# Performance work log

Measured on AMD Instinct MI355X. Metric: run time of the kernel, lower is better.

Reference implementation:

```python
import jax, jax.numpy as jnp
import numpy as np

REG_COEF = 25.0


def setup_inputs() -> dict:
    key = jax.random.key(0)
    k1, k2, k3, k4 = jax.random.split(key, 4)
    B, C, N, RES = 32, 4, 16384, 32
    y_pred = jax.random.normal(k1, (B, C, 4), dtype=jnp.float32)
    points = jax.random.uniform(k2, (B, N, 3), dtype=jnp.float32)  # unit cube
    voxel_grid = jax.random.uniform(k3, (B, RES, RES, RES), dtype=jnp.float32)
    voxel_grid_cp = jax.random.uniform(k4, (B, RES, RES, RES, 3), dtype=jnp.float32)
    return {"y_pred": y_pred, "points": points, "voxel_grid": voxel_grid,
            "voxel_grid_cp": voxel_grid_cp}


def _sym_loss(y_pred, points, voxel_grid, voxel_grid_cp):
    B, C, _ = y_pred.shape
    res = voxel_grid_cp.shape[1]
    normals = y_pred[:, :, 0:3]                       # [B,C,3]
    n_hat = normals / jnp.linalg.norm(normals, axis=-1, keepdims=True)
    d = y_pred[:, :, 3]                               # [B,C]

    # --- regularization loss: ||N N^T - I||_F per batch item, then mean ---
    gram = jnp.einsum('bcd,bed->bce', n_hat, n_hat) - jnp.eye(C, dtype=y_pred.dtype)
    reg_loss = jnp.linalg.norm(gram, axis=(1, 2))     # [B]

    # --- reflexion loss: reflect points across each plane, gather closest points ---
    # signed distance to plane: points . n_hat + d  -> [B,C,N]
    dist = jnp.einsum('bnd,bcd->bcn', points, n_hat) + d[:, :, None]
    reflected = points[:, None, :, :] - 2.0 * dist[..., None] * n_hat[:, :, None, :]  # [B,C,N,3]

    vox = jnp.clip(jnp.floor(reflected * res), 0, res - 1).astype(jnp.int32)  # [B,C,N,3]
    b_idx = jnp.arange(B)[:, None, None]
    cp = voxel_grid_cp[b_idx, vox[..., 0], vox[..., 1], vox[..., 2]]          # [B,C,N,3]

    per_plane = jnp.linalg.norm(reflected - cp, axis=-1).mean(axis=-1)        # [B,C]
    reflexion_loss = per_plane.sum()

    return jnp.reshape(reflexion_loss + REG_COEF * reg_loss.mean(), (1,))


def reference(y_pred, points, voxel_grid, voxel_grid_cp):
    return _sym_loss(y_pred, points, voxel_grid, voxel_grid_cp)
```

## Files before the change

kernel.cpp:

```cpp
#include <hip/hip_runtime.h>
#include <math.h>

#define B_    32
#define C_    4
#define N_    16384
#define RES_  32

#define BPB   32
#define TPB   256
#define PTS   (N_ / (BPB * TPB))

__global__ __launch_bounds__(TPB) void sym_main(
    const float* __restrict__ y_pred,
    const float* __restrict__ points,
    const float* __restrict__ cp,
    float* __restrict__ partials)
{
  const int b = blockIdx.y;

  const float* yp = y_pred + b * (C_ * 4);
  float nx[C_], ny[C_], nz[C_], dd[C_];
#pragma unroll
  for (int c = 0; c < C_; ++c) {
    float ax = yp[c * 4 + 0];
    float ay = yp[c * 4 + 1];
    float az = yp[c * 4 + 2];
    float inv = 1.0f / sqrtf(ax * ax + ay * ay + az * az);
    nx[c] = ax * inv;
    ny[c] = ay * inv;
    nz[c] = az * inv;
    dd[c] = yp[c * 4 + 3];
  }

  const float* pb  = points + (size_t)b * (N_ * 3);
  const float* cpb = cp + (size_t)b * (RES_ * RES_ * RES_ * 3);

  float acc = 0.0f;
  const int t = blockIdx.x * TPB + threadIdx.x;

#pragma unroll
  for (int k = 0; k < PTS; ++k) {
    const int p = t + k * (BPB * TPB);
    const float px = pb[p * 3 + 0];
    const float py = pb[p * 3 + 1];
    const float pz = pb[p * 3 + 2];
#pragma unroll
    for (int c = 0; c < C_; ++c) {
      float dist = px * nx[c] + py * ny[c] + pz * nz[c] + dd[c];
      float t2 = 2.0f * dist;
      float rx = px - t2 * nx[c];
      float ry = py - t2 * ny[c];
      float rz = pz - t2 * nz[c];
      int vx = (int)fminf(fmaxf(floorf(rx * (float)RES_), 0.0f), (float)(RES_ - 1));
      int vy = (int)fminf(fmaxf(floorf(ry * (float)RES_), 0.0f), (float)(RES_ - 1));
      int vz = (int)fminf(fmaxf(floorf(rz * (float)RES_), 0.0f), (float)(RES_ - 1));
      int idx = ((vx * RES_ + vy) * RES_ + vz) * 3;
      float cx = cpb[idx + 0];
      float cy = cpb[idx + 1];
      float cz = cpb[idx + 2];
      float dx = rx - cx;
      float dy = ry - cy;
      float dz = rz - cz;
      acc += sqrtf(dx * dx + dy * dy + dz * dz);
    }
  }

#pragma unroll
  for (int off = 32; off > 0; off >>= 1)
    acc += __shfl_down(acc, off, 64);

  __shared__ float sred[TPB / 64];
  const int lane = threadIdx.x & 63;
  const int wave = threadIdx.x >> 6;
  if (lane == 0) sred[wave] = acc;
  __syncthreads();
  if (threadIdx.x == 0) {
    float tot = 0.0f;
#pragma unroll
    for (int w = 0; w < TPB / 64; ++w) tot += sred[w];
    partials[b * BPB + blockIdx.x] = tot;
  }
}

__global__ __launch_bounds__(256) void sym_final(
    const float* __restrict__ y_pred,
    const float* __restrict__ partials,
    float* __restrict__ out)
{
  __shared__ double sd[256];
  double acc = 0.0;
  for (int i = threadIdx.x; i < B_ * BPB; i += 256)
    acc += (double)partials[i];
  acc *= (1.0 / (double)N_);

  if (threadIdx.x < B_) {
    const int b = threadIdx.x;
    const float* yp = y_pred + b * (C_ * 4);
    float nh[C_][3];
#pragma unroll
    for (int c = 0; c < C_; ++c) {
      float ax = yp[c * 4 + 0];
      float ay = yp[c * 4 + 1];
      float az = yp[c * 4 + 2];
      float inv = 1.0f / sqrtf(ax * ax + ay * ay + az * az);
      nh[c][0] = ax * inv;
      nh[c][1] = ay * inv;
      nh[c][2] = az * inv;
    }
    float s = 0.0f;
#pragma unroll
    for (int c = 0; c < C_; ++c) {
#pragma unroll
      for (int e = 0; e < C_; ++e) {
        float dot = nh[c][0] * nh[e][0] + nh[c][1] * nh[e][1] + nh[c][2] * nh[e][2];
        float g = dot - ((c == e) ? 1.0f : 0.0f);
        s += g * g;
      }
    }
    acc += (25.0 / (double)B_) * (double)sqrtf(s);
  }

  sd[threadIdx.x] = acc;
  __syncthreads();
  for (int off = 128; off > 0; off >>= 1) {
    if (threadIdx.x < off) sd[threadIdx.x] += sd[threadIdx.x + off];
    __syncthreads();
  }
  if (threadIdx.x == 0) out[0] = (float)sd[0];
}

extern "C" void kernel_launch(void* const* d_in, const int* in_sizes, int n_in,
                              void* d_out, int out_size, void* d_ws, size_t ws_size,
                              hipStream_t stream) {
  const float* y_pred = (const float*)d_in[0];
  const float* points = (const float*)d_in[1];
  const float* cp     = (const float*)d_in[3];
  float* partials = (float*)d_ws;
  float* out = (float*)d_out;

  sym_main<<<dim3(BPB, B_), TPB, 0, stream>>>(y_pred, points, cp, partials);
  sym_final<<<1, 256, 0, stream>>>(y_pred, partials, out);
}
```

Before: 83.98 us.

## Remap blocks so each batch's blocks share an XCD and batch gathers

Replaces the 2D grid with a 1D grid whose block id is decoded so that every block of a given batch item lands on the same XCD, assuming round-robin block-to-XCD dispatch. The aim is to keep each batch's voxel_grid_cp working set in one XCD's L2 rather than spread across all eight. It also splits the loop so all reflections and indices are computed first, then all gathers issue together, then the distances are reduced with four accumulators, exposing more memory-level parallelism. This raises register use per thread and depends on the hardware's dispatch order, which is not guaranteed.

```diff
diff --git a/kernel.cpp b/kernel.cpp
--- a/kernel.cpp
+++ b/kernel.cpp
@@ -6,9 +6,10 @@
 #define N_    16384
 #define RES_  32
 
-#define BPB   32
-#define TPB   256
-#define PTS   (N_ / (BPB * TPB))
+#define CHUNKS 32
+#define TPB    256
+#define PTS    (N_ / (CHUNKS * TPB))
+#define NGATH  (PTS * C_)
 
 __global__ __launch_bounds__(TPB) void sym_main(
     const float* __restrict__ y_pred,
@@ -16,7 +17,11 @@
     const float* __restrict__ cp,
     float* __restrict__ partials)
 {
-  const int b = blockIdx.y;
+  const int id   = blockIdx.x;
+  const int xcd  = id & 7;
+  const int slot = id >> 3;
+  const int b     = xcd + 8 * (slot & 3);
+  const int chunk = slot >> 2;
 
   const float* yp = y_pred + b * (C_ * 4);
   float nx[C_], ny[C_], nz[C_], dd[C_];
@@ -35,35 +40,53 @@
   const float* pb  = points + (size_t)b * (N_ * 3);
   const float* cpb = cp + (size_t)b * (RES_ * RES_ * RES_ * 3);
 
-  float acc = 0.0f;
-  const int t = blockIdx.x * TPB + threadIdx.x;
+  const int t = chunk * TPB + threadIdx.x;
 
+  float rx[NGATH], ry[NGATH], rz[NGATH];
+  int lin[NGATH];
 #pragma unroll
   for (int k = 0; k < PTS; ++k) {
-    const int p = t + k * (BPB * TPB);
+    const int p = t + k * (CHUNKS * TPB);
     const float px = pb[p * 3 + 0];
     const float py = pb[p * 3 + 1];
     const float pz = pb[p * 3 + 2];
 #pragma unroll
     for (int c = 0; c < C_; ++c) {
+      const int g = k * C_ + c;
       float dist = px * nx[c] + py * ny[c] + pz * nz[c] + dd[c];
       float t2 = 2.0f * dist;
-      float rx = px - t2 * nx[c];
-      float ry = py - t2 * ny[c];
-      float rz = pz - t2 * nz[c];
-      int vx = (int)fminf(fmaxf(floorf(rx * (float)RES_), 0.0f), (float)(RES_ - 1));
-      int vy = (int)fminf(fmaxf(floorf(ry * (float)RES_), 0.0f), (float)(RES_ - 1));
-      int vz = (int)fminf(fmaxf(floorf(rz * (float)RES_), 0.0f), (float)(RES_ - 1));
-      int idx = ((vx * RES_ + vy) * RES_ + vz) * 3;
-      float cx = cpb[idx + 0];
-      float cy = cpb[idx + 1];
-      float cz = cpb[idx + 2];
-      float dx = rx - cx;
-      float dy = ry - cy;
-      float dz = rz - cz;
-      acc += sqrtf(dx * dx + dy * dy + dz * dz);
+      float x = px - t2 * nx[c];
+      float y = py - t2 * ny[c];
+      float z = pz - t2 * nz[c];
+      rx[g] = x; ry[g] = y; rz[g] = z;
+      int vx = (int)fminf(fmaxf(floorf(x * (float)RES_), 0.0f), (float)(RES_ - 1));
+      int vy = (int)fminf(fmaxf(floorf(y * (float)RES_), 0.0f), (float)(RES_ - 1));
+      int vz = (int)fminf(fmaxf(floorf(z * (float)RES_), 0.0f), (float)(RES_ - 1));
+      lin[g] = ((vx * RES_ + vy) * RES_ + vz) * 3;
     }
   }
+
+  float cx[NGATH], cy[NGATH], cz[NGATH];
+#pragma unroll
+  for (int g = 0; g < NGATH; ++g) {
+    cx[g] = cpb[lin[g] + 0];
+    cy[g] = cpb[lin[g] + 1];
+    cz[g] = cpb[lin[g] + 2];
+  }
+
+  float a0 = 0.0f, a1 = 0.0f, a2 = 0.0f, a3 = 0.0f;
+#pragma unroll
+  for (int g = 0; g < NGATH; g += 4) {
+    float dx0 = rx[g+0] - cx[g+0], dy0 = ry[g+0] - cy[g+0], dz0 = rz[g+0] - cz[g+0];
+    float dx1 = rx[g+1] - cx[g+1], dy1 = ry[g+1] - cy[g+1], dz1 = rz[g+1] - cz[g+1];
+    float dx2 = rx[g+2] - cx[g+2], dy2 = ry[g+2] - cy[g+2], dz2 = rz[g+2] - cz[g+2];
+    float dx3 = rx[g+3] - cx[g+3], dy3 = ry[g+3] - cy[g+3], dz3 = rz[g+3] - cz[g+3];
+    a0 += sqrtf(dx0 * dx0 + dy0 * dy0 + dz0 * dz0);
+    a1 += sqrtf(dx1 * dx1 + dy1 * dy1 + dz1 * dz1);
+    a2 += sqrtf(dx2 * dx2 + dy2 * dy2 + dz2 * dz2);
+    a3 += sqrtf(dx3 * dx3 + dy3 * dy3 + dz3 * dz3);
+  }
+  float acc = (a0 + a1) + (a2 + a3);
 
 #pragma unroll
   for (int off = 32; off > 0; off >>= 1)
@@ -78,7 +101,7 @@
     float tot = 0.0f;
 #pragma unroll
     for (int w = 0; w < TPB / 64; ++w) tot += sred[w];
-    partials[b * BPB + blockIdx.x] = tot;
+    partials[b * CHUNKS + chunk] = tot;
   }
 }
 
@@ -89,7 +112,7 @@
 {
   __shared__ double sd[256];
   double acc = 0.0;
-  for (int i = threadIdx.x; i < B_ * BPB; i += 256)
+  for (int i = threadIdx.x; i < B_ * CHUNKS; i += 256)
     acc += (double)partials[i];
   acc *= (1.0 / (double)N_);
 
@@ -138,6 +161,6 @@
   float* partials = (float*)d_ws;
   float* out = (float*)d_out;
 
-  sym_main<<<dim3(BPB, B_), TPB, 0, stream>>>(y_pred, points, cp, partials);
+  sym_main<<<B_ * CHUNKS, TPB, 0, stream>>>(y_pred, points, cp, partials);
   sym_final<<<1, 256, 0, stream>>>(y_pred, partials, out);
 }
```

New measurement: 81.37 us. 1.03x faster.
